# Kernel tuning notes

Hardware: AMD Instinct MI355X
Metric: run time of the kernel (lower is better)

The kernel has to match this reference:

```python
import jax, jax.numpy as jnp
import numpy as np

D_MODEL = 384
HEAD_SIZE = 64
B, T = 64, 512


def setup_inputs() -> dict:
    key = jax.random.key(0)
    kx, kq, kk, kv = jax.random.split(key, 4)
    x = jax.random.normal(kx, (B, T, D_MODEL), dtype=jnp.float32)
    Wq = jax.random.normal(kq, (D_MODEL, HEAD_SIZE), dtype=jnp.float32) * 0.02
    Wk = jax.random.normal(kk, (D_MODEL, HEAD_SIZE), dtype=jnp.float32) * 0.02
    Wv = jax.random.normal(kv, (D_MODEL, HEAD_SIZE), dtype=jnp.float32) * 0.02
    return {"x": x, "Wq": Wq, "Wk": Wk, "Wv": Wv}


def reference(x, Wq, Wk, Wv):
    # x: [B, T, C]; projections (bias-free linear layers)
    q = jnp.einsum("btc,ch->bth", x, Wq)  # [B, T, H]
    k = jnp.einsum("btc,ch->bth", x, Wk)
    v = jnp.einsum("btc,ch->bth", x, Wv)
    Tn = x.shape[1]
    scale = 1.0 / jnp.sqrt(jnp.float32(k.shape[-1]))
    wei = jnp.einsum("bqh,bkh->bqk", q, k) * scale  # [B, T, T]
    causal = jnp.tril(jnp.ones((Tn, Tn), dtype=bool))
    wei = jnp.where(causal, wei, -jnp.inf)
    wei = jax.nn.softmax(wei, axis=-1)
    # dropout omitted (eval mode) for deterministic reference
    out = jnp.einsum("bqk,bkh->bqh", wei, v)  # [B, T, H]
    return out
```

## Files before the change

kernel.cpp:

```cpp
#include <hip/hip_runtime.h>
#include <math.h>

#define NB 64
#define NT 512
#define NC 384
#define NH 64

typedef __attribute__((ext_vector_type(8))) short bf16x8;
typedef __attribute__((ext_vector_type(4))) float f32x4;

__device__ __forceinline__ unsigned short f2bf(float f) {
  unsigned int u = __float_as_uint(f);
  return (unsigned short)((u + 0x7FFFu + ((u >> 16) & 1u)) >> 16);
}
__device__ __forceinline__ unsigned int cvt_pk_bf16(float lo, float hi) {
  unsigned int r;
  asm("v_cvt_pk_bf16_f32 %0, %1, %2" : "=v"(r) : "v"(lo), "v"(hi));
  return r;
}

__global__ __launch_bounds__(256) void wtrans_kernel(
    const float* __restrict__ Wq, const float* __restrict__ Wk,
    const float* __restrict__ Wv, unsigned short* __restrict__ Wt) {
  int id = blockIdx.x * 256 + threadIdx.x;
  if (id >= 3 * NC * NH) return;
  int m = id / (NC * NH);
  int r = id % (NC * NH);
  int c = r / NH;
  int h = r % NH;
  const float* W = (m == 0) ? Wq : ((m == 1) ? Wk : Wv);
  Wt[(m * NH + h) * NC + c] = f2bf(W[c * NH + h]);
}

#define XS 392
__global__ __launch_bounds__(384, 6) void proj_kernel(
    const float* __restrict__ x, const unsigned short* __restrict__ Wt,
    unsigned short* __restrict__ q, unsigned short* __restrict__ k,
    unsigned short* __restrict__ vt) {
  __shared__ unsigned short xs[32 * XS];
  const int t = threadIdx.x;
  const int m0 = blockIdx.x * 32;
  const int w = t / 64, l = t & 63, mi = l & 15, quad = l >> 4;

#pragma unroll
  for (int i = 0; i < 8; ++i) {
    int u = t + i * 384;
    int row = u / 96;
    int cp = (u % 96) * 4;
    float4 a = *(const float4*)(x + (size_t)(m0 + row) * NC + cp);
    uint2 bbu;
    bbu.x = cvt_pk_bf16(a.x, a.y);
    bbu.y = cvt_pk_bf16(a.z, a.w);
    *(uint2*)&xs[row * XS + cp] = bbu;
  }
  __syncthreads();

  f32x4 acc[2][2];
  const f32x4 zero = {0.f, 0.f, 0.f, 0.f};
#pragma unroll
  for (int i = 0; i < 2; ++i)
#pragma unroll
    for (int j = 0; j < 2; ++j) acc[i][j] = zero;

  const unsigned short* wr0 = Wt + (size_t)((w * 2 + 0) * 16 + mi) * NC + quad * 8;
  const unsigned short* wr1 = Wt + (size_t)((w * 2 + 1) * 16 + mi) * NC + quad * 8;

#pragma unroll
  for (int kc = 0; kc < 12; ++kc) {
    bf16x8 b0 = *(const bf16x8*)(wr0 + kc * 32);
    bf16x8 b1 = *(const bf16x8*)(wr1 + kc * 32);
#pragma unroll
    for (int msub = 0; msub < 2; ++msub) {
      bf16x8 a = *(const bf16x8*)&xs[(msub * 16 + mi) * XS + kc * 32 + quad * 8];
      acc[0][msub] =
          __builtin_amdgcn_mfma_f32_16x16x32_bf16(a, b0, acc[0][msub], 0, 0, 0);
      acc[1][msub] =
          __builtin_amdgcn_mfma_f32_16x16x32_bf16(a, b1, acc[1][msub], 0, 0, 0);
    }
  }

  if (w < 4) {
    unsigned short* dst = (w < 2) ? q : k;
    const float sc = (w < 2) ? 0.125f : 1.0f;
#pragma unroll
    for (int ntl = 0; ntl < 2; ++ntl) {
      int tile = w * 2 + ntl;
      int h = (tile & 3) * 16 + mi;
#pragma unroll
      for (int msub = 0; msub < 2; ++msub) {
        unsigned int u01 =
            cvt_pk_bf16(acc[ntl][msub][0] * sc, acc[ntl][msub][1] * sc);
        unsigned int u23 =
            cvt_pk_bf16(acc[ntl][msub][2] * sc, acc[ntl][msub][3] * sc);
        size_t base = (size_t)(m0 + msub * 16 + quad * 4) * NH + h;
        dst[base] = (unsigned short)u01;
        dst[base + NH] = (unsigned short)(u01 >> 16);
        dst[base + 2 * NH] = (unsigned short)u23;
        dst[base + 3 * NH] = (unsigned short)(u23 >> 16);
      }
    }
  } else {
    int bb = m0 >> 9, t0 = m0 & 511;
#pragma unroll
    for (int ntl = 0; ntl < 2; ++ntl) {
      int tile = w * 2 + ntl;
      int h = (tile & 3) * 16 + mi;
#pragma unroll
      for (int msub = 0; msub < 2; ++msub) {
        uint2 s_;
        s_.x = cvt_pk_bf16(acc[ntl][msub][0], acc[ntl][msub][1]);
        s_.y = cvt_pk_bf16(acc[ntl][msub][2], acc[ntl][msub][3]);
        *(uint2*)&vt[((size_t)bb * NH + h) * NT + t0 + msub * 16 + quad * 4] = s_;
      }
    }
  }
}

#define PSTR 72
__global__ __launch_bounds__(64, 2) void attn_kernel(
    const unsigned short* __restrict__ q, const unsigned short* __restrict__ k,
    const unsigned short* __restrict__ vt, float* __restrict__ out) {
  __shared__ unsigned short ps[16 * PSTR];
  __shared__ __align__(16) float alpha_s[16];
  const int l = threadIdx.x;
  const int mi = l & 15, quad = l >> 4;
  const int bx = blockIdx.x;
  const int qi = 31 - (bx >> 6);
  const int b = bx & 63;

  const unsigned short* qrow = q + ((size_t)b * NT + qi * 16 + mi) * NH;
  bf16x8 qb0 = *(const bf16x8*)(qrow + quad * 8);
  bf16x8 qb1 = *(const bf16x8*)(qrow + 32 + quad * 8);

  f32x4 accO[4];
  const f32x4 zero = {0.f, 0.f, 0.f, 0.f};
#pragma unroll
  for (int i = 0; i < 4; ++i) accO[i] = zero;
  float mrow = -INFINITY, lrow = 0.f;

  const unsigned short* kbase = k + (size_t)b * NT * NH;
  const unsigned short* vbase = vt + (size_t)b * NH * NT;
  const int ktmax = (qi * 16 + 15) >> 6;

  bf16x8 ka0A[4], ka1A[4], va0A[4], va1A[4];
  bf16x8 ka0B[4], ka1B[4], va0B[4], va1B[4];

#define LOADKV(KA0, KA1, VA0, VA1, KT)                                        \
  {                                                                           \
    const unsigned short* kb_ = kbase + (size_t)(KT) * 64 * NH;               \
    const unsigned short* vb_ = vbase + (KT) * 64;                            \
    _Pragma("unroll") for (int nt_ = 0; nt_ < 4; ++nt_) {                     \
      const unsigned short* kr_ =                                             \
          kb_ + (size_t)(nt_ * 16 + mi) * NH + quad * 8;                      \
      KA0[nt_] = *(const bf16x8*)kr_;                                         \
      KA1[nt_] = *(const bf16x8*)(kr_ + 32);                                  \
      const unsigned short* vr_ =                                             \
          vb_ + (size_t)(nt_ * 16 + mi) * NT + quad * 8;                      \
      VA0[nt_] = *(const bf16x8*)vr_;                                         \
      VA1[nt_] = *(const bf16x8*)(vr_ + 32);                                  \
    }                                                                         \
  }

#define COMPUTE(KA0, KA1, VA0, VA1, KT)                                       \
  {                                                                           \
                         \
    float p_[4][4];                                                           \
    _Pragma("unroll") for (int nt_ = 0; nt_ < 4; ++nt_) {                     \
      f32x4 z_ = zero;                                                        \
      z_ = __builtin_amdgcn_mfma_f32_16x16x32_bf16(KA0[nt_], qb0, z_, 0, 0, 0); \
      z_ = __builtin_amdgcn_mfma_f32_16x16x32_bf16(KA1[nt_], qb1, z_, 0, 0, 0); \
      _Pragma("unroll") for (int r_ = 0; r_ < 4; ++r_) p_[nt_][r_] = z_[r_];  \
    }                                                                         \
    if ((KT) == ktmax) {                    \
      _Pragma("unroll") for (int nt_ = 0; nt_ < 4; ++nt_)                     \
          _Pragma("unroll") for (int r_ = 0; r_ < 4; ++r_)                    \
              if ((KT)*64 + nt_ * 16 + quad * 4 + r_ > qi * 16 + mi)          \
        p_[nt_][r_] = -INFINITY;                                              \
    }                                                                         \
    float vmax_ = -INFINITY;                                                  \
    _Pragma("unroll") for (int nt_ = 0; nt_ < 4; ++nt_)                       \
        _Pragma("unroll") for (int r_ = 0; r_ < 4; ++r_)                      \
            vmax_ = fmaxf(vmax_, p_[nt_][r_]);                                \
    vmax_ = fmaxf(vmax_, __shfl_xor(vmax_, 16));                              \
    vmax_ = fmaxf(vmax_, __shfl_xor(vmax_, 32));                              \
    float mn_ = fmaxf(mrow, vmax_);                                           \
    float alpha_ = __expf(mrow - mn_);                                        \
    mrow = mn_;                                                               \
    float rsum_ = 0.f;                                                        \
    _Pragma("unroll") for (int nt_ = 0; nt_ < 4; ++nt_)                       \
        _Pragma("unroll") for (int r_ = 0; r_ < 4; ++r_) {                    \
      p_[nt_][r_] = __expf(p_[nt_][r_] - mn_);                                \
      rsum_ += p_[nt_][r_];                                                   \
    }                                                                         \
    rsum_ += __shfl_xor(rsum_, 16);                                           \
    rsum_ += __shfl_xor(rsum_, 32);                                           \
    lrow = lrow * alpha_ + rsum_;                                             \
                     \
    if (quad == 0) alpha_s[mi] = alpha_;                                      \
    _Pragma("unroll") for (int nt_ = 0; nt_ < 4; ++nt_) {                     \
      uint2 pk_;                                                              \
      pk_.x = cvt_pk_bf16(p_[nt_][0], p_[nt_][1]);                            \
      pk_.y = cvt_pk_bf16(p_[nt_][2], p_[nt_][3]);                            \
      *(uint2*)&ps[mi * PSTR + nt_ * 16 + quad * 4] = pk_;                    \
    }                                                                         \
    bf16x8 pa0_ = *(const bf16x8*)&ps[mi * PSTR + quad * 8];                  \
    bf16x8 pa1_ = *(const bf16x8*)&ps[mi * PSTR + 32 + quad * 8];             \
    f32x4 av_ = *(const f32x4*)&alpha_s[quad * 4];                            \
    _Pragma("unroll") for (int hi_ = 0; hi_ < 4; ++hi_)                       \
        _Pragma("unroll") for (int r_ = 0; r_ < 4; ++r_)                      \
            accO[hi_][r_] *= av_[r_];                                         \
                    \
    _Pragma("unroll") for (int hi_ = 0; hi_ < 4; ++hi_) {                     \
      accO[hi_] = __builtin_amdgcn_mfma_f32_16x16x32_bf16(pa0_, VA0[hi_],     \
                                                          accO[hi_], 0, 0, 0); \
      accO[hi_] = __builtin_amdgcn_mfma_f32_16x16x32_bf16(pa1_, VA1[hi_],     \
                                                          accO[hi_], 0, 0, 0); \
    }                                                                         \
  }

  LOADKV(ka0A, ka1A, va0A, va1A, 0);
  int kt = 0;
  while (kt < ktmax) {
    LOADKV(ka0B, ka1B, va0B, va1B, kt + 1);
    COMPUTE(ka0A, ka1A, va0A, va1A, kt);
    ++kt;
    if (kt < ktmax) {
      LOADKV(ka0A, ka1A, va0A, va1A, kt + 1);
      COMPUTE(ka0B, ka1B, va0B, va1B, kt);
      ++kt;
    } else {
      COMPUTE(ka0B, ka1B, va0B, va1B, kt);
      ++kt;
    }
  }
  if (kt == ktmax) COMPUTE(ka0A, ka1A, va0A, va1A, kt);

  float inv = 1.f / lrow;
  if (quad == 0) alpha_s[mi] = inv;
  f32x4 iv4 = *(const f32x4*)&alpha_s[quad * 4];
  const size_t obase = ((size_t)b * NT + qi * 16) * NH;
#pragma unroll
  for (int r = 0; r < 4; ++r) {
#pragma unroll
    for (int hi = 0; hi < 4; ++hi)
      out[obase + (size_t)(quad * 4 + r) * NH + hi * 16 + mi] =
          accO[hi][r] * iv4[r];
  }
#undef LOADKV
#undef COMPUTE
}

extern "C" void kernel_launch(void* const* d_in, const int* in_sizes, int n_in,
                              void* d_out, int out_size, void* d_ws, size_t ws_size,
                              hipStream_t stream) {
  const float* x  = (const float*)d_in[0];
  const float* Wq = (const float*)d_in[1];
  const float* Wk = (const float*)d_in[2];
  const float* Wv = (const float*)d_in[3];

  unsigned short* Wt = (unsigned short*)d_ws;
  unsigned short* qb = Wt + 192 * 384;
  unsigned short* kb = qb + 32768 * 64;
  unsigned short* vtb = kb + 32768 * 64;
  float* out = (float*)d_out;

  wtrans_kernel<<<288, 256, 0, stream>>>(Wq, Wk, Wv, Wt);
  proj_kernel<<<1024, 384, 0, stream>>>(x, Wt, qb, kb, vtb);
  attn_kernel<<<2048, 64, 0, stream>>>(qb, kb, vtb, out);
}
```

Baseline: 126.3 us.

## Process two row tiles per projection block with register-prefetched x loads

Each projection block now handles 64 rows instead of 32, split into two halves with separate shared-memory buffers. The second half's x data is loaded into registers before the first half's MFMA compute, so global load latency overlaps with compute. The grid is halved and launch bounds are lowered to 3 blocks per CU, trading occupancy and more registers for fewer blocks and better latency hiding.

```diff
diff --git a/kernel.cpp b/kernel.cpp
--- a/kernel.cpp
+++ b/kernel.cpp
@@ -33,87 +33,111 @@
 }
 
 #define XS 392
-__global__ __launch_bounds__(384, 6) void proj_kernel(
+__global__ __launch_bounds__(384, 3) void proj_kernel(
     const float* __restrict__ x, const unsigned short* __restrict__ Wt,
     unsigned short* __restrict__ q, unsigned short* __restrict__ k,
     unsigned short* __restrict__ vt) {
-  __shared__ unsigned short xs[32 * XS];
+  __shared__ unsigned short xs[2][32 * XS];
   const int t = threadIdx.x;
-  const int m0 = blockIdx.x * 32;
+  const int m0 = blockIdx.x * 64;
   const int w = t / 64, l = t & 63, mi = l & 15, quad = l >> 4;
 
-#pragma unroll
-  for (int i = 0; i < 8; ++i) {
-    int u = t + i * 384;
-    int row = u / 96;
-    int cp = (u % 96) * 4;
-    float4 a = *(const float4*)(x + (size_t)(m0 + row) * NC + cp);
+  const unsigned short* wr0 =
+      Wt + (size_t)((w * 2 + 0) * 16 + mi) * NC + quad * 8;
+  const unsigned short* wr1 =
+      Wt + (size_t)((w * 2 + 1) * 16 + mi) * NC + quad * 8;
+
+  float4 xr[8];
+#pragma unroll
+  for (int i = 0; i < 8; ++i) {
+    int u = t + i * 384;
+    xr[i] = *(const float4*)(x + (size_t)(m0 + u / 96) * NC + (u % 96) * 4);
+  }
+#pragma unroll
+  for (int i = 0; i < 8; ++i) {
+    int u = t + i * 384;
     uint2 bbu;
-    bbu.x = cvt_pk_bf16(a.x, a.y);
-    bbu.y = cvt_pk_bf16(a.z, a.w);
-    *(uint2*)&xs[row * XS + cp] = bbu;
+    bbu.x = cvt_pk_bf16(xr[i].x, xr[i].y);
+    bbu.y = cvt_pk_bf16(xr[i].z, xr[i].w);
+    *(uint2*)&xs[0][(u / 96) * XS + (u % 96) * 4] = bbu;
   }
   __syncthreads();
 
-  f32x4 acc[2][2];
-  const f32x4 zero = {0.f, 0.f, 0.f, 0.f};
-#pragma unroll
-  for (int i = 0; i < 2; ++i)
-#pragma unroll
-    for (int j = 0; j < 2; ++j) acc[i][j] = zero;
-
-  const unsigned short* wr0 = Wt + (size_t)((w * 2 + 0) * 16 + mi) * NC + quad * 8;
-  const unsigned short* wr1 = Wt + (size_t)((w * 2 + 1) * 16 + mi) * NC + quad * 8;
-
-#pragma unroll
-  for (int kc = 0; kc < 12; ++kc) {
-    bf16x8 b0 = *(const bf16x8*)(wr0 + kc * 32);
-    bf16x8 b1 = *(const bf16x8*)(wr1 + kc * 32);
-#pragma unroll
-    for (int msub = 0; msub < 2; ++msub) {
-      bf16x8 a = *(const bf16x8*)&xs[(msub * 16 + mi) * XS + kc * 32 + quad * 8];
-      acc[0][msub] =
-          __builtin_amdgcn_mfma_f32_16x16x32_bf16(a, b0, acc[0][msub], 0, 0, 0);
-      acc[1][msub] =
-          __builtin_amdgcn_mfma_f32_16x16x32_bf16(a, b1, acc[1][msub], 0, 0, 0);
-    }
-  }
-
-  if (w < 4) {
-    unsigned short* dst = (w < 2) ? q : k;
-    const float sc = (w < 2) ? 0.125f : 1.0f;
-#pragma unroll
-    for (int ntl = 0; ntl < 2; ++ntl) {
-      int tile = w * 2 + ntl;
-      int h = (tile & 3) * 16 + mi;
-#pragma unroll
-      for (int msub = 0; msub < 2; ++msub) {
-        unsigned int u01 =
-            cvt_pk_bf16(acc[ntl][msub][0] * sc, acc[ntl][msub][1] * sc);
-        unsigned int u23 =
-            cvt_pk_bf16(acc[ntl][msub][2] * sc, acc[ntl][msub][3] * sc);
-        size_t base = (size_t)(m0 + msub * 16 + quad * 4) * NH + h;
-        dst[base] = (unsigned short)u01;
-        dst[base + NH] = (unsigned short)(u01 >> 16);
-        dst[base + 2 * NH] = (unsigned short)u23;
-        dst[base + 3 * NH] = (unsigned short)(u23 >> 16);
-      }
-    }
-  } else {
-    int bb = m0 >> 9, t0 = m0 & 511;
-#pragma unroll
-    for (int ntl = 0; ntl < 2; ++ntl) {
-      int tile = w * 2 + ntl;
-      int h = (tile & 3) * 16 + mi;
-#pragma unroll
-      for (int msub = 0; msub < 2; ++msub) {
-        uint2 s_;
-        s_.x = cvt_pk_bf16(acc[ntl][msub][0], acc[ntl][msub][1]);
-        s_.y = cvt_pk_bf16(acc[ntl][msub][2], acc[ntl][msub][3]);
-        *(uint2*)&vt[((size_t)bb * NH + h) * NT + t0 + msub * 16 + quad * 4] = s_;
-      }
-    }
-  }
+#pragma unroll
+  for (int i = 0; i < 8; ++i) {
+    int u = t + i * 384;
+    xr[i] =
+        *(const float4*)(x + (size_t)(m0 + 32 + u / 96) * NC + (u % 96) * 4);
+  }
+
+#define COMPUTE_HALF(HH)                                                      \
+  {                                                                           \
+    f32x4 acc[2][2];                                           \
+    const f32x4 zero_ = {0.f, 0.f, 0.f, 0.f};                                 \
+    _Pragma("unroll") for (int i_ = 0; i_ < 2; ++i_)                          \
+        _Pragma("unroll") for (int j_ = 0; j_ < 2; ++j_) acc[i_][j_] = zero_; \
+    _Pragma("unroll") for (int kc_ = 0; kc_ < 12; ++kc_) {                    \
+      bf16x8 b0_ = *(const bf16x8*)(wr0 + kc_ * 32);                          \
+      bf16x8 b1_ = *(const bf16x8*)(wr1 + kc_ * 32);                          \
+      _Pragma("unroll") for (int ms_ = 0; ms_ < 2; ++ms_) {                   \
+        bf16x8 a_ = *(const bf16x8*)&xs[HH][(ms_ * 16 + mi) * XS + kc_ * 32 + \
+                                           quad * 8];                         \
+        acc[0][ms_] = __builtin_amdgcn_mfma_f32_16x16x32_bf16(a_, b0_,        \
+                                                              acc[0][ms_],   \
+                                                              0, 0, 0);       \
+        acc[1][ms_] = __builtin_amdgcn_mfma_f32_16x16x32_bf16(a_, b1_,        \
+                                                              acc[1][ms_],   \
+                                                              0, 0, 0);       \
+      }                                                                       \
+    }                                                                         \
+                    \
+    if (w < 4) {                           \
+      unsigned short* dst_ = (w < 2) ? q : k;                                 \
+      const float sc_ = (w < 2) ? 0.125f : 1.0f;                              \
+      _Pragma("unroll") for (int ntl_ = 0; ntl_ < 2; ++ntl_) {                \
+        int hcol_ = ((w * 2 + ntl_) & 3) * 16 + mi;                           \
+        _Pragma("unroll") for (int ms_ = 0; ms_ < 2; ++ms_) {                 \
+          unsigned int u01_ = cvt_pk_bf16(acc[ntl_][ms_][0] * sc_,            \
+                                          acc[ntl_][ms_][1] * sc_);           \
+          unsigned int u23_ = cvt_pk_bf16(acc[ntl_][ms_][2] * sc_,            \
+                                          acc[ntl_][ms_][3] * sc_);           \
+          size_t base_ =                                                      \
+              (size_t)(m0 + (HH)*32 + ms_ * 16 + quad * 4) * NH + hcol_;      \
+          dst_[base_] = (unsigned short)u01_;                                 \
+          dst_[base_ + NH] = (unsigned short)(u01_ >> 16);                    \
+          dst_[base_ + 2 * NH] = (unsigned short)u23_;                        \
+          dst_[base_ + 3 * NH] = (unsigned short)(u23_ >> 16);                \
+        }                                                                     \
+      }                                                                       \
+    } else {    \
+      int bb_ = m0 >> 9, t0_ = m0 & 511;                                      \
+      _Pragma("unroll") for (int ntl_ = 0; ntl_ < 2; ++ntl_) {                \
+        int hcol_ = ((w * 2 + ntl_) & 3) * 16 + mi;                           \
+        _Pragma("unroll") for (int ms_ = 0; ms_ < 2; ++ms_) {                 \
+          uint2 s_;                                                           \
+          s_.x = cvt_pk_bf16(acc[ntl_][ms_][0], acc[ntl_][ms_][1]);           \
+          s_.y = cvt_pk_bf16(acc[ntl_][ms_][2], acc[ntl_][ms_][3]);           \
+          *(uint2*)&vt[((size_t)bb_ * NH + hcol_) * NT + t0_ + (HH)*32 +      \
+                       ms_ * 16 + quad * 4] = s_;                             \
+        }                                                                     \
+      }                                                                       \
+    }                                                                         \
+  }
+
+  COMPUTE_HALF(0)
+
+#pragma unroll
+  for (int i = 0; i < 8; ++i) {
+    int u = t + i * 384;
+    uint2 bbu;
+    bbu.x = cvt_pk_bf16(xr[i].x, xr[i].y);
+    bbu.y = cvt_pk_bf16(xr[i].z, xr[i].w);
+    *(uint2*)&xs[1][(u / 96) * XS + (u % 96) * 4] = bbu;
+  }
+  __syncthreads();
+
+  COMPUTE_HALF(1)
+#undef COMPUTE_HALF
 }
 
 #define PSTR 72
@@ -265,6 +289,6 @@
   float* out = (float*)d_out;
 
   wtrans_kernel<<<288, 256, 0, stream>>>(Wq, Wk, Wv, Wt);
-  proj_kernel<<<1024, 384, 0, stream>>>(x, Wt, qb, kb, vtb);
+  proj_kernel<<<512, 384, 0, stream>>>(x, Wt, qb, kb, vtb);
   attn_kernel<<<2048, 64, 0, stream>>>(qb, kb, vtb, out);
 }
```

After: 128.1 us. No clear change (+1.4%).
